# Performance work log

Hardware: AMD Instinct MI355X
Metric: run time of the kernel (lower is better)

The kernel has to match this reference:

```python
import jax, jax.numpy as jnp
import numpy as np

X_SCALE = 20.0
THR = 0.25
BETA = 15.0
DT = 1.0
GAIN = 1.0


def setup_inputs() -> dict:
    key = jax.random.key(0)
    k1, k2, k3 = jax.random.split(key, 3)
    x = jax.random.normal(k1, (32, 1, 8192), dtype=jnp.float32)
    conv_w = jax.random.normal(k2, (64, 1, 8), dtype=jnp.float32)
    raw_tau = jax.random.normal(k3, (64,), dtype=jnp.float32)
    return {"x": x, "conv_w": conv_w, "raw_tau": raw_tau}


def _forward(x, conv_w, raw_tau):
    K = conv_w.shape[-1]
    # normalize each filter to unit norm (clamp_min 1e-8)
    norms = jnp.linalg.norm(conv_w.reshape(conv_w.shape[0], -1), axis=1)
    w = conv_w / jnp.maximum(norms, 1e-8)[:, None, None]
    # causal conv: left-pad by K-1
    I = GAIN * jax.lax.conv_general_dilated(
        X_SCALE * x, w, window_strides=(1,), padding=[(K - 1, 0)],
        dimension_numbers=("NCH", "OIH", "NCH"))  # (B, F, L)
    tau = jax.nn.softplus(raw_tau) + 1e-4
    alpha = jnp.exp(-DT / tau).astype(I.dtype)  # (F,)

    def step(v, I_t):
        v_pre = alpha * v + (1.0 - alpha) * I_t  # (B, F)
        z = BETA * (v_pre - THR)
        s = (v_pre >= THR).astype(I_t.dtype)  # hard spike, no grad
        v_new = v_pre * (1.0 - s)  # reset where spiked
        return v_new, (z, s)

    I_tfirst = jnp.transpose(I, (2, 0, 1))  # (L, B, F)
    v0 = jnp.zeros(I.shape[:2], dtype=I.dtype)  # (B, F)
    _, (z, s) = jax.lax.scan(step, v0, I_tfirst)
    z = jnp.transpose(z, (1, 2, 0))  # (B, F, L)
    s = jnp.transpose(s, (1, 2, 0))
    logits = jnp.max(z, axis=1)  # (B, L)
    return I, z, s, logits


def reference(x, conv_w, raw_tau):
    return _forward(x, conv_w, raw_tau)
```

## Files before the change

kernel.cpp:

```cpp
#include <hip/hip_runtime.h>
#include <math.h>


#define LL 8192
#define BB 32
#define FF 64
#define KK 8
#define CHUNK 64
#define NCH 128
#define WARM 64
#define NX (WARM + KK - 1 + CHUNK)
#define TS 32
#define NT (CHUNK / TS)

typedef float vfloat4 __attribute__((ext_vector_type(4)));

__global__ __launch_bounds__(64) void snn_kernel(
    const float* __restrict__ x, const float* __restrict__ conv_w,
    const float* __restrict__ raw_tau, float* __restrict__ out)
{
    __shared__ float x_lds[NX + 1];
    __shared__ float I_tile[FF][TS + 1];
    __shared__ float z_tile[FF][TS + 1];

    const int f  = threadIdx.x;
    const int b  = blockIdx.y;
    const int c  = blockIdx.x;
    const int t0 = c * CHUNK;
    const int g0 = t0 - WARM - (KK - 1);

    double wd[KK];
    double ss = 0.0;
    #pragma unroll
    for (int k = 0; k < KK; ++k) {
        double wv = (double)conv_w[f * KK + k];
        wd[k] = wv;
        ss += wv * wv;
    }
    double nrm = sqrt(ss);
    if (nrm < 1e-8) nrm = 1e-8;
    double invn = 1.0 / nrm;
    float wf[KK];
    #pragma unroll
    for (int k = 0; k < KK; ++k) wf[k] = (float)(wd[k] * invn);

    double rt    = (double)raw_tau[f];
    double tau   = log1p(exp(rt)) + 1e-4;
    float alpha  = (float)exp(-1.0 / tau);
    float oma    = 1.0f - alpha;

    for (int i = f; i < NX; i += 64) {
        int g = g0 + i;
        x_lds[i] = (g >= 0) ? (20.0f * x[(size_t)b * LL + g]) : 0.0f;
    }
    __syncthreads();

    float* outI  = out;
    float* outZ  = out + (size_t)BB * FF * LL;
    float* outS  = out + (size_t)2 * BB * FF * LL;
    float* outLg = out + (size_t)3 * BB * FF * LL;

    float v = 0.0f;

    #pragma unroll 8
    for (int s = 0; s < WARM; ++s) {
        float acc = 0.0f;
        #pragma unroll
        for (int k = 0; k < KK; ++k) acc = fmaf(wf[k], x_lds[s + k], acc);
        float vp = fmaf(alpha, v, oma * acc);
        v = (vp >= 0.25f) ? 0.0f : vp;
    }

    for (int tile = 0; tile < NT; ++tile) {
        #pragma unroll
        for (int j = 0; j < TS; ++j) {
            int s = WARM + tile * TS + j;
            float acc = 0.0f;
            #pragma unroll
            for (int k = 0; k < KK; ++k) acc = fmaf(wf[k], x_lds[s + k], acc);
            float vp = fmaf(alpha, v, oma * acc);
            I_tile[f][j] = acc;
            z_tile[f][j] = 15.0f * (vp - 0.25f);
            v = (vp >= 0.25f) ? 0.0f : vp;
        }
        __syncthreads();

        const int gt = t0 + tile * TS;
        {
            int r = f >> 3;
            int q = (f & 7) * 4;
            vfloat4 vi[8], vz[8];
            #pragma unroll
            for (int it = 0; it < 8; ++it) {
                int fr = it * 8 + r;
                vi[it] = (vfloat4){I_tile[fr][q], I_tile[fr][q + 1],
                                   I_tile[fr][q + 2], I_tile[fr][q + 3]};
                vz[it] = (vfloat4){z_tile[fr][q], z_tile[fr][q + 1],
                                   z_tile[fr][q + 2], z_tile[fr][q + 3]};
            }
            #pragma unroll
            for (int it = 0; it < 8; ++it) {
                size_t base = ((size_t)b * FF + it * 8 + r) * LL + gt + q;
                __builtin_nontemporal_store(vi[it], (vfloat4*)(outI + base));
            }
            #pragma unroll
            for (int it = 0; it < 8; ++it) {
                size_t base = ((size_t)b * FF + it * 8 + r) * LL + gt + q;
                __builtin_nontemporal_store(vz[it], (vfloat4*)(outZ + base));
            }
            #pragma unroll
            for (int it = 0; it < 8; ++it) {
                vfloat4 zz = vz[it];
                vfloat4 vs = {zz.x >= 0.f ? 1.f : 0.f,
                              zz.y >= 0.f ? 1.f : 0.f,
                              zz.z >= 0.f ? 1.f : 0.f,
                              zz.w >= 0.f ? 1.f : 0.f};
                size_t base = ((size_t)b * FF + it * 8 + r) * LL + gt + q;
                __builtin_nontemporal_store(vs, (vfloat4*)(outS + base));
            }
            if (f < TS) {
                float m = z_tile[0][f];
                #pragma unroll
                for (int ff = 1; ff < FF; ++ff) m = fmaxf(m, z_tile[ff][f]);
                outLg[(size_t)b * LL + gt + f] = m;
            }
        }
        __syncthreads();
    }
}

extern "C" void kernel_launch(void* const* d_in, const int* in_sizes, int n_in,
                              void* d_out, int out_size, void* d_ws, size_t ws_size,
                              hipStream_t stream) {
    const float* x  = (const float*)d_in[0];
    const float* w  = (const float*)d_in[1];
    const float* rt = (const float*)d_in[2];
    float* out = (float*)d_out;
    dim3 grid(NCH, BB);
    snn_kernel<<<grid, 64, 0, stream>>>(x, w, rt, out);
}
```

Measured before the change: 212.5 us.

## Halve chunk size, recompute conv in store phase, keep x window in registers

Each block now covers 32 timesteps instead of 64, which doubles the grid to 256x32 blocks. The 64-step warm-up is still run per block, so the share of redundant warm-up work grows. The conv input window now slides through registers instead of being re-read from LDS on every step. The I tile in LDS is removed; the store phase recomputes the convolution from weights staged in LDS, and only z is staged through LDS. The aim is more parallelism, less LDS traffic and fewer barriers, in exchange for more warm-up recompute per output.

```diff
diff --git a/kernel.cpp b/kernel.cpp
--- a/kernel.cpp
+++ b/kernel.cpp
@@ -6,12 +6,10 @@
 #define BB 32
 #define FF 64
 #define KK 8
-#define CHUNK 64
-#define NCH 128
+#define CHUNK 32
+#define NCH (LL / CHUNK)
 #define WARM 64
-#define NX (WARM + KK - 1 + CHUNK)
-#define TS 32
-#define NT (CHUNK / TS)
+#define NX (WARM + KK - 1 + CHUNK + 1)
 
 typedef float vfloat4 __attribute__((ext_vector_type(4)));
 
@@ -19,30 +17,28 @@
     const float* __restrict__ x, const float* __restrict__ conv_w,
     const float* __restrict__ raw_tau, float* __restrict__ out)
 {
-    __shared__ float x_lds[NX + 1];
-    __shared__ float I_tile[FF][TS + 1];
-    __shared__ float z_tile[FF][TS + 1];
+    __shared__ float x_lds[NX];
+    __shared__ float w_lds[FF][KK];
+    __shared__ float z_tile[FF][CHUNK + 1];
 
     const int f  = threadIdx.x;
+    const int c  = blockIdx.x;
     const int b  = blockIdx.y;
-    const int c  = blockIdx.x;
     const int t0 = c * CHUNK;
     const int g0 = t0 - WARM - (KK - 1);
 
-    double wd[KK];
-    double ss = 0.0;
+    double wd[KK]; double ss = 0.0;
     #pragma unroll
     for (int k = 0; k < KK; ++k) {
-        double wv = (double)conv_w[f * KK + k];
-        wd[k] = wv;
-        ss += wv * wv;
+        wd[k] = (double)conv_w[f * KK + k];
+        ss += wd[k] * wd[k];
     }
     double nrm = sqrt(ss);
     if (nrm < 1e-8) nrm = 1e-8;
     double invn = 1.0 / nrm;
     float wf[KK];
     #pragma unroll
-    for (int k = 0; k < KK; ++k) wf[k] = (float)(wd[k] * invn);
+    for (int k = 0; k < KK; ++k) { wf[k] = (float)(wd[k] * invn); w_lds[f][k] = wf[k]; }
 
     double rt    = (double)raw_tau[f];
     double tau   = log1p(exp(rt)) + 1e-4;
@@ -51,7 +47,37 @@
 
     for (int i = f; i < NX; i += 64) {
         int g = g0 + i;
-        x_lds[i] = (g >= 0) ? (20.0f * x[(size_t)b * LL + g]) : 0.0f;
+        x_lds[i] = (g >= 0 && g < LL) ? (20.0f * x[(size_t)b * LL + g]) : 0.0f;
+    }
+    __syncthreads();
+
+    float xw[KK];
+    #pragma unroll
+    for (int k = 0; k < KK; ++k) xw[k] = x_lds[k];
+    float v = 0.0f;
+
+    #pragma unroll 8
+    for (int s = 0; s < WARM; ++s) {
+        float acc = 0.0f;
+        #pragma unroll
+        for (int k = 0; k < KK; ++k) acc = fmaf(wf[k], xw[k], acc);
+        float vp = fmaf(alpha, v, oma * acc);
+        v = (vp >= 0.25f) ? 0.0f : vp;
+        #pragma unroll
+        for (int k = 0; k < KK - 1; ++k) xw[k] = xw[k + 1];
+        xw[KK - 1] = x_lds[s + KK];
+    }
+    #pragma unroll 8
+    for (int j = 0; j < CHUNK; ++j) {
+        float acc = 0.0f;
+        #pragma unroll
+        for (int k = 0; k < KK; ++k) acc = fmaf(wf[k], xw[k], acc);
+        float vp = fmaf(alpha, v, oma * acc);
+        z_tile[f][j] = 15.0f * (vp - 0.25f);
+        v = (vp >= 0.25f) ? 0.0f : vp;
+        #pragma unroll
+        for (int k = 0; k < KK - 1; ++k) xw[k] = xw[k + 1];
+        xw[KK - 1] = x_lds[WARM + j + KK];
     }
     __syncthreads();
 
@@ -60,72 +86,40 @@
     float* outS  = out + (size_t)2 * BB * FF * LL;
     float* outLg = out + (size_t)3 * BB * FF * LL;
 
-    float v = 0.0f;
+    const int r = f >> 3;
+    const int q = (f & 7) * 4;
 
-    #pragma unroll 8
-    for (int s = 0; s < WARM; ++s) {
-        float acc = 0.0f;
+    float xv[KK + 3];
+    #pragma unroll
+    for (int m = 0; m < KK + 3; ++m) xv[m] = x_lds[WARM + q + m];
+
+    #pragma unroll
+    for (int it = 0; it < 8; ++it) {
+        const int fr = it * 8 + r;
+        float wl[KK];
         #pragma unroll
-        for (int k = 0; k < KK; ++k) acc = fmaf(wf[k], x_lds[s + k], acc);
-        float vp = fmaf(alpha, v, oma * acc);
-        v = (vp >= 0.25f) ? 0.0f : vp;
+        for (int k = 0; k < KK; ++k) wl[k] = w_lds[fr][k];
+        vfloat4 vi, vz, vs;
+        #pragma unroll
+        for (int i = 0; i < 4; ++i) {
+            float a = 0.0f;
+            #pragma unroll
+            for (int k = 0; k < KK; ++k) a = fmaf(wl[k], xv[i + k], a);
+            vi[i] = a;
+            float zz = z_tile[fr][q + i];
+            vz[i] = zz;
+            vs[i] = (zz >= 0.0f) ? 1.0f : 0.0f;
+        }
+        size_t base = ((size_t)b * FF + fr) * LL + t0 + q;
+        __builtin_nontemporal_store(vi, (vfloat4*)(outI + base));
+        __builtin_nontemporal_store(vz, (vfloat4*)(outZ + base));
+        __builtin_nontemporal_store(vs, (vfloat4*)(outS + base));
     }
-
-    for (int tile = 0; tile < NT; ++tile) {
+    if (f < CHUNK) {
+        float m = z_tile[0][f];
         #pragma unroll
-        for (int j = 0; j < TS; ++j) {
-            int s = WARM + tile * TS + j;
-            float acc = 0.0f;
-            #pragma unroll
-            for (int k = 0; k < KK; ++k) acc = fmaf(wf[k], x_lds[s + k], acc);
-            float vp = fmaf(alpha, v, oma * acc);
-            I_tile[f][j] = acc;
-            z_tile[f][j] = 15.0f * (vp - 0.25f);
-            v = (vp >= 0.25f) ? 0.0f : vp;
-        }
-        __syncthreads();
-
-        const int gt = t0 + tile * TS;
-        {
-            int r = f >> 3;
-            int q = (f & 7) * 4;
-            vfloat4 vi[8], vz[8];
-            #pragma unroll
-            for (int it = 0; it < 8; ++it) {
-                int fr = it * 8 + r;
-                vi[it] = (vfloat4){I_tile[fr][q], I_tile[fr][q + 1],
-                                   I_tile[fr][q + 2], I_tile[fr][q + 3]};
-                vz[it] = (vfloat4){z_tile[fr][q], z_tile[fr][q + 1],
-                                   z_tile[fr][q + 2], z_tile[fr][q + 3]};
-            }
-            #pragma unroll
-            for (int it = 0; it < 8; ++it) {
-                size_t base = ((size_t)b * FF + it * 8 + r) * LL + gt + q;
-                __builtin_nontemporal_store(vi[it], (vfloat4*)(outI + base));
-            }
-            #pragma unroll
-            for (int it = 0; it < 8; ++it) {
-                size_t base = ((size_t)b * FF + it * 8 + r) * LL + gt + q;
-                __builtin_nontemporal_store(vz[it], (vfloat4*)(outZ + base));
-            }
-            #pragma unroll
-            for (int it = 0; it < 8; ++it) {
-                vfloat4 zz = vz[it];
-                vfloat4 vs = {zz.x >= 0.f ? 1.f : 0.f,
-                              zz.y >= 0.f ? 1.f : 0.f,
-                              zz.z >= 0.f ? 1.f : 0.f,
-                              zz.w >= 0.f ? 1.f : 0.f};
-                size_t base = ((size_t)b * FF + it * 8 + r) * LL + gt + q;
-                __builtin_nontemporal_store(vs, (vfloat4*)(outS + base));
-            }
-            if (f < TS) {
-                float m = z_tile[0][f];
-                #pragma unroll
-                for (int ff = 1; ff < FF; ++ff) m = fmaxf(m, z_tile[ff][f]);
-                outLg[(size_t)b * LL + gt + f] = m;
-            }
-        }
-        __syncthreads();
+        for (int ff = 1; ff < FF; ++ff) m = fmaxf(m, z_tile[ff][f]);
+        outLg[(size_t)b * LL + t0 + f] = m;
     }
 }
 
```

Result: no change. 214.6 us (+1.0%).
